# Optimization experiments

Hardware: AMD Instinct MI355X
Metric: run time of the kernel (lower is better)

The kernel has to match this reference:

```python
import jax, jax.numpy as jnp
import numpy as np

SIZE = 1024
M = 10            # log2(SIZE); number of butterfly factors
N_TERMS = 10
BATCH = 8192

# diagonal offset of butterfly j (order matches torch: range(m)[::-1])
DIAGS = [1 << (M - 1 - j) for j in range(M)]


def setup_inputs() -> dict:
    key = jax.random.key(0)
    k1, k2, k3, k4, k5 = jax.random.split(key, 5)
    x = jax.random.normal(k1, (BATCH, SIZE), dtype=jnp.float32)
    diag = jax.random.normal(k2, (M, SIZE), dtype=jnp.float32)
    subpad = jax.random.normal(k3, (M, SIZE), dtype=jnp.float32)
    suppad = jax.random.normal(k4, (M, SIZE), dtype=jnp.float32)
    logit = jax.random.normal(k5, (N_TERMS, M), dtype=jnp.float32)
    # zero the padded positions: subdiag has length SIZE-d stored in [d:],
    # superdiag has length SIZE-d stored in [:-d]
    idx = np.arange(SIZE)
    sub_mask = np.stack([idx >= d for d in DIAGS]).astype(np.float32)
    sup_mask = np.stack([idx < SIZE - d for d in DIAGS]).astype(np.float32)
    subpad = subpad * jnp.asarray(sub_mask)
    suppad = suppad * jnp.asarray(sup_mask)
    return {"x": x, "diag": diag, "subpad": subpad, "suppad": suppad, "logit": logit}


def _butterfly(x, dg, sb, sp, d):
    # out = dg*x; out[d:] += subdiag*x[:-d]; out[:-d] += superdiag*x[d:]
    z = jnp.zeros(x.shape[:-1] + (d,), x.dtype)
    x_right = jnp.concatenate([z, x[..., :-d]], axis=-1)  # x shifted right by d
    x_left = jnp.concatenate([x[..., d:], z], axis=-1)    # x shifted left by d
    return dg * x + sb * x_right + sp * x_left


def reference(x, diag, subpad, suppad, logit):
    prob = jax.nn.softmax(logit, axis=-1)  # (n_terms, m)
    out = x
    for i in range(N_TERMS)[::-1]:
        # apply all m butterflies to current output, stack on last dim
        ys = jnp.stack(
            [_butterfly(out, diag[j], subpad[j], suppad[j], DIAGS[j]) for j in range(M)],
            axis=-1,
        )  # (..., size, m)
        out = jnp.einsum('bsm,m->bs', ys, prob[i])
    return out
```

## Files before the change

### kernel.cpp

```cpp
#include <hip/hip_runtime.h>

#define SIZE 1024
#define MM 10
#define NTERMS 10

typedef _Float16 f16;
typedef __attribute__((ext_vector_type(8))) _Float16 f16x8;
typedef __attribute__((ext_vector_type(4))) _Float16 f16x4;
typedef __attribute__((ext_vector_type(4))) float    f32x4;
typedef __attribute__((ext_vector_type(2))) int      i2;

typedef const __attribute__((address_space(1))) _Float16 gf16;
typedef __attribute__((address_space(3))) _Float16 sf16;

__device__ __forceinline__ float4 ldq(const float* p) { return *(const float4*)p; }

#define FMA4F(W, v0, v1, v2, v3)                                     \
    a0 = fmaf((W)[0], (v0), a0); a1 = fmaf((W)[1], (v1), a1);        \
    a2 = fmaf((W)[2], (v2), a2); a3 = fmaf((W)[3], (v3), a3);

__device__ __forceinline__ void cvt16(const float4& v0, const float4& v1, f16x8& h) {
    h[0] = (f16)v0.x; h[1] = (f16)v0.y; h[2] = (f16)v0.z; h[3] = (f16)v0.w;
    h[4] = (f16)v1.x; h[5] = (f16)v1.y; h[6] = (f16)v1.z; h[7] = (f16)v1.w;
}

__global__ __launch_bounds__(256, 2)
void fused_pre(const float* __restrict__ x,
               const float* __restrict__ diag,
               const float* __restrict__ subpad,
               const float* __restrict__ suppad,
               const float* __restrict__ logit,
               f16* __restrict__ Gt,
               f16* __restrict__ xh)
{
    __shared__ float buf[2][2][SIZE];

    const int tid = threadIdx.x;

    if (blockIdx.x >= 512) {
        const long i = ((long)(blockIdx.x - 512) * 256 + tid) * 16;
        const float4 a = ldq(x + i), b = ldq(x + i + 4),
                     c = ldq(x + i + 8), d = ldq(x + i + 12);
        f16x8 h0, h1; cvt16(a, b, h0); cvt16(c, d, h1);
        *(f16x8*)(xh + i)     = h0;
        *(f16x8*)(xh + i + 8) = h1;
        return;
    }

    const int s0  = tid * 4;
    const int rowbase = blockIdx.x * 2;

    #pragma unroll
    for (int r = 0; r < 2; ++r) {
        float4 v;
        v.x = (rowbase + r == s0 + 0) ? 1.f : 0.f;
        v.y = (rowbase + r == s0 + 1) ? 1.f : 0.f;
        v.z = (rowbase + r == s0 + 2) ? 1.f : 0.f;
        v.w = (rowbase + r == s0 + 3) ? 1.f : 0.f;
        *(float4*)&buf[0][r][s0] = v;
    }
    __syncthreads();

    int cur = 0;
    for (int t = 0; t < NTERMS; ++t) {
        const int i = NTERMS - 1 - t;

        float lg[MM];
        float mx = -3.4e38f;
        #pragma unroll
        for (int j = 0; j < MM; ++j) { lg[j] = logit[i * MM + j]; mx = fmaxf(mx, lg[j]); }
        float ssum = 0.f;
        #pragma unroll
        for (int j = 0; j < MM; ++j) { lg[j] = __expf(lg[j] - mx); ssum += lg[j]; }
        const float inv = 1.0f / ssum;

        float D[4] = {0.f, 0.f, 0.f, 0.f};
        float Wsb[MM][4], Wsp[MM][4];
        #pragma unroll
        for (int j = 0; j < MM; ++j) {
            const float pj = lg[j] * inv;
            const float4 dg = ldq(diag   + j * SIZE + s0);
            const float4 sb = ldq(subpad + j * SIZE + s0);
            const float4 sp = ldq(suppad + j * SIZE + s0);
            D[0] = fmaf(pj, dg.x, D[0]); D[1] = fmaf(pj, dg.y, D[1]);
            D[2] = fmaf(pj, dg.z, D[2]); D[3] = fmaf(pj, dg.w, D[3]);
            Wsb[j][0] = pj * sb.x; Wsb[j][1] = pj * sb.y;
            Wsb[j][2] = pj * sb.z; Wsb[j][3] = pj * sb.w;
            Wsp[j][0] = pj * sp.x; Wsp[j][1] = pj * sp.y;
            Wsp[j][2] = pj * sp.z; Wsp[j][3] = pj * sp.w;
        }

        const bool last = (t == NTERMS - 1);
        for (int r = 0; r < 2; ++r) {
            const float* row = &buf[cur][r][0];

            const float4 xo = ldq(row + s0);
            float a0 = D[0] * xo.x, a1 = D[1] * xo.y,
                  a2 = D[2] * xo.z, a3 = D[3] * xo.w;

            const float4 xl = ldq(row + (s0 >= 4         ? s0 - 4 : 0));
            const float4 xr = ldq(row + (s0 + 4 <= 1020  ? s0 + 4 : 1020));

            FMA4F(Wsb[9], xl.w, xo.x, xo.y, xo.z)
            FMA4F(Wsp[9], xo.y, xo.z, xo.w, xr.x)
            FMA4F(Wsb[8], xl.z, xl.w, xo.x, xo.y)
            FMA4F(Wsp[8], xo.z, xo.w, xr.x, xr.y)
            FMA4F(Wsb[7], xl.x, xl.y, xl.z, xl.w)
            FMA4F(Wsp[7], xr.x, xr.y, xr.z, xr.w)
            #pragma unroll
            for (int j = 0; j <= 6; ++j) {
                const int d = 512 >> j;
                const float4 xm = ldq(row + (s0 >= d        ? s0 - d : 0));
                const float4 xp = ldq(row + (s0 + d <= 1020 ? s0 + d : 1020));
                FMA4F(Wsb[j], xm.x, xm.y, xm.z, xm.w)
                FMA4F(Wsp[j], xp.x, xp.y, xp.z, xp.w)
            }

            if (last) {
                const int k = rowbase + r;
                Gt[(long)(s0 + 0) * SIZE + k] = (f16)a0;
                Gt[(long)(s0 + 1) * SIZE + k] = (f16)a1;
                Gt[(long)(s0 + 2) * SIZE + k] = (f16)a2;
                Gt[(long)(s0 + 3) * SIZE + k] = (f16)a3;
            } else {
                *(float4*)&buf[cur ^ 1][r][s0] = make_float4(a0, a1, a2, a3);
            }
        }
        __syncthreads();
        cur ^= 1;
    }
}

#define NKT 32

__global__ __launch_bounds__(64)
void gemm64(const f16* __restrict__ xh,
            const f16* __restrict__ Gt,
            float* __restrict__ out)
{
    __shared__ f16 Xs[2][64][32];

    const int lane = threadIdx.x;
    const int bm   = blockIdx.x & 127;
    const int bn   = blockIdx.x >> 7;
    const int lr   = lane & 15, lk = lane >> 4;

    const f16* gsrc = xh + (long)(bm * 64 + (lane >> 2)) * 1024 + (lane & 3) * 8;

    const f16* gbase = Gt + (long)(bn * 64 + lr) * 1024 + lk * 8;

    f32x4 acc[4][4];
    #pragma unroll
    for (int mi = 0; mi < 4; ++mi)
        #pragma unroll
        for (int ni = 0; ni < 4; ++ni)
            acc[mi][ni] = (f32x4){0.f, 0.f, 0.f, 0.f};

    f16x8 b0, b1, b2, b3;
    f16x8 c0, c1, c2, c3;

#define STAGE(BUF, KT) {                                                      \
        const f16* gp = gsrc + (KT) * 32;                                     \
        sf16* lp = (sf16*)&Xs[BUF][0][0];                                     \
        __builtin_amdgcn_global_load_lds((gf16*)gp,               lp,        16, 0, 0); \
        __builtin_amdgcn_global_load_lds((gf16*)(gp + 16 * 1024), lp +  512, 16, 0, 0); \
        __builtin_amdgcn_global_load_lds((gf16*)(gp + 32 * 1024), lp + 1024, 16, 0, 0); \
        __builtin_amdgcn_global_load_lds((gf16*)(gp + 48 * 1024), lp + 1536, 16, 0, 0); }
#define LOAD_B(B0, B1, B2, B3, KT) {                                  \
        const f16* gp = gbase + (KT) * 32;                            \
        B0 = *(const f16x8*)(gp);                                     \
        B1 = *(const f16x8*)(gp + 16 * 1024);                         \
        B2 = *(const f16x8*)(gp + 32 * 1024);                         \
        B3 = *(const f16x8*)(gp + 48 * 1024); }
#define COMPUTE(BUF, B0, B1, B2, B3) {                                \
        f16x8 a0 = *(const f16x8*)&Xs[BUF][ 0 + lr][lk * 8];          \
        f16x8 a1 = *(const f16x8*)&Xs[BUF][16 + lr][lk * 8];          \
        f16x8 a2 = *(const f16x8*)&Xs[BUF][32 + lr][lk * 8];          \
        f16x8 a3 = *(const f16x8*)&Xs[BUF][48 + lr][lk * 8];          \
        acc[0][0] = __builtin_amdgcn_mfma_f32_16x16x32_f16(a0, B0, acc[0][0], 0, 0, 0); \
        acc[0][1] = __builtin_amdgcn_mfma_f32_16x16x32_f16(a0, B1, acc[0][1], 0, 0, 0); \
        acc[0][2] = __builtin_amdgcn_mfma_f32_16x16x32_f16(a0, B2, acc[0][2], 0, 0, 0); \
        acc[0][3] = __builtin_amdgcn_mfma_f32_16x16x32_f16(a0, B3, acc[0][3], 0, 0, 0); \
        acc[1][0] = __builtin_amdgcn_mfma_f32_16x16x32_f16(a1, B0, acc[1][0], 0, 0, 0); \
        acc[1][1] = __builtin_amdgcn_mfma_f32_16x16x32_f16(a1, B1, acc[1][1], 0, 0, 0); \
        acc[1][2] = __builtin_amdgcn_mfma_f32_16x16x32_f16(a1, B2, acc[1][2], 0, 0, 0); \
        acc[1][3] = __builtin_amdgcn_mfma_f32_16x16x32_f16(a1, B3, acc[1][3], 0, 0, 0); \
        acc[2][0] = __builtin_amdgcn_mfma_f32_16x16x32_f16(a2, B0, acc[2][0], 0, 0, 0); \
        acc[2][1] = __builtin_amdgcn_mfma_f32_16x16x32_f16(a2, B1, acc[2][1], 0, 0, 0); \
        acc[2][2] = __builtin_amdgcn_mfma_f32_16x16x32_f16(a2, B2, acc[2][2], 0, 0, 0); \
        acc[2][3] = __builtin_amdgcn_mfma_f32_16x16x32_f16(a2, B3, acc[2][3], 0, 0, 0); \
        acc[3][0] = __builtin_amdgcn_mfma_f32_16x16x32_f16(a3, B0, acc[3][0], 0, 0, 0); \
        acc[3][1] = __builtin_amdgcn_mfma_f32_16x16x32_f16(a3, B1, acc[3][1], 0, 0, 0); \
        acc[3][2] = __builtin_amdgcn_mfma_f32_16x16x32_f16(a3, B2, acc[3][2], 0, 0, 0); \
        acc[3][3] = __builtin_amdgcn_mfma_f32_16x16x32_f16(a3, B3, acc[3][3], 0, 0, 0); }

    STAGE(0, 0); LOAD_B(b0, b1, b2, b3, 0);
    __syncthreads();

    #pragma unroll 1
    for (int kt2 = 0; kt2 < NKT / 2; ++kt2) {
        const int kt = kt2 * 2;
        STAGE(1, kt + 1);
        LOAD_B(c0, c1, c2, c3, kt + 1);
        COMPUTE(0, b0, b1, b2, b3);
        __syncthreads();
        if (kt2 < NKT / 2 - 1) {
            STAGE(0, kt + 2);
            LOAD_B(b0, b1, b2, b3, kt + 2);
        }
        COMPUTE(1, c0, c1, c2, c3);
        __syncthreads();
    }

    const long orow0 = (long)bm * 64 + lk * 4;
    const int  ocol0 = bn * 64 + lr;
    #pragma unroll
    for (int mi = 0; mi < 4; ++mi)
        #pragma unroll
        for (int ni = 0; ni < 4; ++ni)
            #pragma unroll
            for (int q = 0; q < 4; ++q)
                out[(orow0 + mi * 16 + q) * 1024 + ocol0 + ni * 16] = acc[mi][ni][q];

#undef STAGE
#undef LOAD_B
#undef COMPUTE
}

#define RPB 16
#define MIX_L(acc, r32, ww) \
    asm("v_fma_mix_f32 %0, %1, %2, %0 op_sel:[0,0,0] op_sel_hi:[1,0,0]" \
        : "+v"(acc) : "v"(r32), "v"(ww))
#define MIX_H(acc, r32, ww) \
    asm("v_fma_mix_f32 %0, %1, %2, %0 op_sel:[1,0,0] op_sel_hi:[1,0,0]" \
        : "+v"(acc) : "v"(r32), "v"(ww))

__global__ __launch_bounds__(256, 2)
void butterfly_h16mix(const float* __restrict__ x,
                      const float* __restrict__ diag,
                      const float* __restrict__ subpad,
                      const float* __restrict__ suppad,
                      const float* __restrict__ logit,
                      float* __restrict__ out)
{
    __shared__ f16 buf[2][RPB][SIZE];
    const int tid = threadIdx.x;
    const int s0  = tid * 4;
    const long rowbase = (long)blockIdx.x * RPB;

    #pragma unroll
    for (int r = 0; r < RPB; ++r) {
        const float4 v = ldq(x + (rowbase + r) * SIZE + s0);
        f16x4 h;
        h[0] = (f16)v.x; h[1] = (f16)v.y; h[2] = (f16)v.z; h[3] = (f16)v.w;
        *(f16x4*)&buf[0][r][s0] = h;
    }
    __syncthreads();

    int cur = 0;
    for (int t = 0; t < NTERMS; ++t) {
        const int i = NTERMS - 1 - t;
        float lg[MM];
        float mx = -3.4e38f;
        #pragma unroll
        for (int j = 0; j < MM; ++j) { lg[j] = logit[i * MM + j]; mx = fmaxf(mx, lg[j]); }
        float ssum = 0.f;
        #pragma unroll
        for (int j = 0; j < MM; ++j) { lg[j] = __expf(lg[j] - mx); ssum += lg[j]; }
        const float inv = 1.0f / ssum;

        float D[4] = {0.f, 0.f, 0.f, 0.f};
        float Wsb[MM][4], Wsp[MM][4];
        #pragma unroll
        for (int j = 0; j < MM; ++j) {
            const float pj = lg[j] * inv;
            const float4 dg = ldq(diag   + j * SIZE + s0);
            const float4 sb = ldq(subpad + j * SIZE + s0);
            const float4 sp = ldq(suppad + j * SIZE + s0);
            D[0] = fmaf(pj, dg.x, D[0]); D[1] = fmaf(pj, dg.y, D[1]);
            D[2] = fmaf(pj, dg.z, D[2]); D[3] = fmaf(pj, dg.w, D[3]);
            Wsb[j][0] = pj * sb.x; Wsb[j][1] = pj * sb.y;
            Wsb[j][2] = pj * sb.z; Wsb[j][3] = pj * sb.w;
            Wsp[j][0] = pj * sp.x; Wsp[j][1] = pj * sp.y;
            Wsp[j][2] = pj * sp.z; Wsp[j][3] = pj * sp.w;
        }

        const bool last = (t == NTERMS - 1);
        for (int r = 0; r < RPB; ++r) {
            const f16* row = &buf[cur][r][0];
            const i2 xo = *(const i2*)&row[s0];
            const i2 xl = *(const i2*)&row[(s0 >= 4)        ? s0 - 4 : 0];
            const i2 xr = *(const i2*)&row[(s0 + 4 <= 1020) ? s0 + 4 : 1020];
            float a0 = 0.f, a1 = 0.f, a2 = 0.f, a3 = 0.f;

            MIX_L(a0, xo.x, D[0]); MIX_H(a1, xo.x, D[1]);
            MIX_L(a2, xo.y, D[2]); MIX_H(a3, xo.y, D[3]);
            MIX_H(a0, xl.y, Wsb[9][0]); MIX_L(a1, xo.x, Wsb[9][1]);
            MIX_H(a2, xo.x, Wsb[9][2]); MIX_L(a3, xo.y, Wsb[9][3]);
            MIX_H(a0, xo.x, Wsp[9][0]); MIX_L(a1, xo.y, Wsp[9][1]);
            MIX_H(a2, xo.y, Wsp[9][2]); MIX_L(a3, xr.x, Wsp[9][3]);
            MIX_L(a0, xl.y, Wsb[8][0]); MIX_H(a1, xl.y, Wsb[8][1]);
            MIX_L(a2, xo.x, Wsb[8][2]); MIX_H(a3, xo.x, Wsb[8][3]);
            MIX_L(a0, xo.y, Wsp[8][0]); MIX_H(a1, xo.y, Wsp[8][1]);
            MIX_L(a2, xr.x, Wsp[8][2]); MIX_H(a3, xr.x, Wsp[8][3]);
            MIX_L(a0, xl.x, Wsb[7][0]); MIX_H(a1, xl.x, Wsb[7][1]);
            MIX_L(a2, xl.y, Wsb[7][2]); MIX_H(a3, xl.y, Wsb[7][3]);
            MIX_L(a0, xr.x, Wsp[7][0]); MIX_H(a1, xr.x, Wsp[7][1]);
            MIX_L(a2, xr.y, Wsp[7][2]); MIX_H(a3, xr.y, Wsp[7][3]);
            #pragma unroll
            for (int j = 0; j <= 6; ++j) {
                const int d = 512 >> j;
                const i2 xm = *(const i2*)&row[(s0 >= d)        ? s0 - d : 0];
                const i2 xp = *(const i2*)&row[(s0 + d <= 1020) ? s0 + d : 1020];
                MIX_L(a0, xm.x, Wsb[j][0]); MIX_H(a1, xm.x, Wsb[j][1]);
                MIX_L(a2, xm.y, Wsb[j][2]); MIX_H(a3, xm.y, Wsb[j][3]);
                MIX_L(a0, xp.x, Wsp[j][0]); MIX_H(a1, xp.x, Wsp[j][1]);
                MIX_L(a2, xp.y, Wsp[j][2]); MIX_H(a3, xp.y, Wsp[j][3]);
            }

            if (last) {
                *(float4*)(out + (rowbase + r) * SIZE + s0) =
                    make_float4(a0, a1, a2, a3);
            } else {
                f16x4 hv;
                hv[0] = (f16)a0; hv[1] = (f16)a1; hv[2] = (f16)a2; hv[3] = (f16)a3;
                *(f16x4*)&buf[cur ^ 1][r][s0] = hv;
            }
        }
        __syncthreads();
        cur ^= 1;
    }
}

extern "C" void kernel_launch(void* const* d_in, const int* in_sizes, int n_in,
                              void* d_out, int out_size, void* d_ws, size_t ws_size,
                              hipStream_t stream) {
    const float* x      = (const float*)d_in[0];
    const float* diag   = (const float*)d_in[1];
    const float* subpad = (const float*)d_in[2];
    const float* suppad = (const float*)d_in[3];
    const float* logit  = (const float*)d_in[4];
    float* outp = (float*)d_out;

    const int batch = in_sizes[0] / SIZE;
    const size_t needGt = (size_t)SIZE * SIZE * sizeof(f16);
    const size_t needXh = (size_t)batch * SIZE * sizeof(f16);

    if (d_ws != nullptr && ws_size >= needGt + needXh) {
        f16* Gt = (f16*)d_ws;
        f16* xh = (f16*)((char*)d_ws + needGt);
        const int cvtBlocks = (int)(((long)batch * SIZE) / (256 * 16));
        fused_pre<<<dim3(512 + cvtBlocks), dim3(256), 0, stream>>>(
            x, diag, subpad, suppad, logit, Gt, xh);
        const int nblocks = (batch / 64) * (SIZE / 64);
        gemm64<<<dim3(nblocks), dim3(64), 0, stream>>>(xh, Gt, outp);
    } else {
        butterfly_h16mix<<<dim3(batch / RPB), dim3(256), 0, stream>>>(
            x, diag, subpad, suppad, logit, outp);
    }
}
```

Baseline: 82.03 us.

## Triple-buffer gemm64 LDS stages with vmcnt waits instead of barriers

```diff
diff --git a/kernel.cpp b/kernel.cpp
--- a/kernel.cpp
+++ b/kernel.cpp
@@ -138,7 +138,7 @@
             const f16* __restrict__ Gt,
             float* __restrict__ out)
 {
-    __shared__ f16 Xs[2][64][32];
+    __shared__ f16 Xs[3][64][32];
 
     const int lane = threadIdx.x;
     const int bm   = blockIdx.x & 127;
@@ -146,7 +146,6 @@
     const int lr   = lane & 15, lk = lane >> 4;
 
     const f16* gsrc = xh + (long)(bm * 64 + (lane >> 2)) * 1024 + (lane & 3) * 8;
-
     const f16* gbase = Gt + (long)(bn * 64 + lr) * 1024 + lk * 8;
 
     f32x4 acc[4][4];
@@ -156,9 +155,14 @@
         for (int ni = 0; ni < 4; ++ni)
             acc[mi][ni] = (f32x4){0.f, 0.f, 0.f, 0.f};
 
-    f16x8 b0, b1, b2, b3;
-    f16x8 c0, c1, c2, c3;
-
+    f16x8 bE0, bE1, bE2, bE3;
+    f16x8 bO0, bO1, bO2, bO3;
+    f16x8 a0, a1, a2, a3;
+
+#define WAITV8 { asm volatile("s_waitcnt vmcnt(8)" ::: "memory"); \
+                 __builtin_amdgcn_sched_barrier(0); }
+#define WAITV4 { asm volatile("s_waitcnt vmcnt(4)" ::: "memory"); \
+                 __builtin_amdgcn_sched_barrier(0); }
 #define STAGE(BUF, KT) {                                                      \
         const f16* gp = gsrc + (KT) * 32;                                     \
         sf16* lp = (sf16*)&Xs[BUF][0][0];                                     \
@@ -166,17 +170,19 @@
         __builtin_amdgcn_global_load_lds((gf16*)(gp + 16 * 1024), lp +  512, 16, 0, 0); \
         __builtin_amdgcn_global_load_lds((gf16*)(gp + 32 * 1024), lp + 1024, 16, 0, 0); \
         __builtin_amdgcn_global_load_lds((gf16*)(gp + 48 * 1024), lp + 1536, 16, 0, 0); }
-#define LOAD_B(B0, B1, B2, B3, KT) {                                  \
+#define LOADB(B0, B1, B2, B3, KT) {                                   \
         const f16* gp = gbase + (KT) * 32;                            \
         B0 = *(const f16x8*)(gp);                                     \
         B1 = *(const f16x8*)(gp + 16 * 1024);                         \
         B2 = *(const f16x8*)(gp + 32 * 1024);                         \
         B3 = *(const f16x8*)(gp + 48 * 1024); }
-#define COMPUTE(BUF, B0, B1, B2, B3) {                                \
-        f16x8 a0 = *(const f16x8*)&Xs[BUF][ 0 + lr][lk * 8];          \
-        f16x8 a1 = *(const f16x8*)&Xs[BUF][16 + lr][lk * 8];          \
-        f16x8 a2 = *(const f16x8*)&Xs[BUF][32 + lr][lk * 8];          \
-        f16x8 a3 = *(const f16x8*)&Xs[BUF][48 + lr][lk * 8];          \
+#define READA(BUF) {                                                  \
+        const f16* base = (const f16*)&Xs[BUF][0][0];                 \
+        a0 = *(const f16x8*)(base + ( 0 + lr) * 32 + lk * 8);         \
+        a1 = *(const f16x8*)(base + (16 + lr) * 32 + lk * 8);         \
+        a2 = *(const f16x8*)(base + (32 + lr) * 32 + lk * 8);         \
+        a3 = *(const f16x8*)(base + (48 + lr) * 32 + lk * 8); }
+#define MFMA16(B0, B1, B2, B3) {                                      \
         acc[0][0] = __builtin_amdgcn_mfma_f32_16x16x32_f16(a0, B0, acc[0][0], 0, 0, 0); \
         acc[0][1] = __builtin_amdgcn_mfma_f32_16x16x32_f16(a0, B1, acc[0][1], 0, 0, 0); \
         acc[0][2] = __builtin_amdgcn_mfma_f32_16x16x32_f16(a0, B2, acc[0][2], 0, 0, 0); \
@@ -194,23 +200,29 @@
         acc[3][2] = __builtin_amdgcn_mfma_f32_16x16x32_f16(a3, B2, acc[3][2], 0, 0, 0); \
         acc[3][3] = __builtin_amdgcn_mfma_f32_16x16x32_f16(a3, B3, acc[3][3], 0, 0, 0); }
 
-    STAGE(0, 0); LOAD_B(b0, b1, b2, b3, 0);
-    __syncthreads();
+    STAGE(0, 0); STAGE(1, 1); LOADB(bE0, bE1, bE2, bE3, 0);
 
     #pragma unroll 1
-    for (int kt2 = 0; kt2 < NKT / 2; ++kt2) {
+    for (int kt2 = 0; kt2 < 15; ++kt2) {
         const int kt = kt2 * 2;
-        STAGE(1, kt + 1);
-        LOAD_B(c0, c1, c2, c3, kt + 1);
-        COMPUTE(0, b0, b1, b2, b3);
-        __syncthreads();
-        if (kt2 < NKT / 2 - 1) {
-            STAGE(0, kt + 2);
-            LOAD_B(b0, b1, b2, b3, kt + 2);
-        }
-        COMPUTE(1, c0, c1, c2, c3);
-        __syncthreads();
-    }
+        WAITV8;
+        READA(kt % 3);
+        STAGE((kt + 2) % 3, kt + 2);
+        LOADB(bO0, bO1, bO2, bO3, kt + 1);
+        MFMA16(bE0, bE1, bE2, bE3);
+        WAITV8;
+        READA((kt + 1) % 3);
+        STAGE((kt + 3) % 3, kt + 3);
+        LOADB(bE0, bE1, bE2, bE3, kt + 2);
+        MFMA16(bO0, bO1, bO2, bO3);
+    }
+    WAITV8;
+    READA(0);
+    LOADB(bO0, bO1, bO2, bO3, 31);
+    MFMA16(bE0, bE1, bE2, bE3);
+    WAITV4;
+    READA(1);
+    MFMA16(bO0, bO1, bO2, bO3);
 
     const long orow0 = (long)bm * 64 + lk * 4;
     const int  ocol0 = bn * 64 + lr;
@@ -222,9 +234,12 @@
             for (int q = 0; q < 4; ++q)
                 out[(orow0 + mi * 16 + q) * 1024 + ocol0 + ni * 16] = acc[mi][ni][q];
 
+#undef WAITV8
+#undef WAITV4
 #undef STAGE
-#undef LOAD_B
-#undef COMPUTE
+#undef LOADB
+#undef READA
+#undef MFMA16
 }
 
 #define RPB 16
```

Result: slower. 83.70 us (+2.0%).

## Use 4-wave 128x128x64 GEMM tiles with XOR-swizzled shared-memory A tiles

Applied to the files above, without the earlier changes.

```diff
diff --git a/kernel.cpp b/kernel.cpp
--- a/kernel.cpp
+++ b/kernel.cpp
@@ -131,23 +131,31 @@
     }
 }
 
-#define NKT 32
-
-__global__ __launch_bounds__(64)
-void gemm64(const f16* __restrict__ xh,
-            const f16* __restrict__ Gt,
-            float* __restrict__ out)
+#define BMT 128
+#define BNT 128
+#define BKT 64
+#define NKT (1024 / BKT)
+
+__global__ __launch_bounds__(256, 2)
+void gemm_f16(const f16* __restrict__ xh,
+              const f16* __restrict__ Gt,
+              float* __restrict__ out)
 {
-    __shared__ f16 Xs[2][64][32];
-
-    const int lane = threadIdx.x;
-    const int bm   = blockIdx.x & 127;
-    const int bn   = blockIdx.x >> 7;
+    __shared__ f16 Xs[2][BMT][BKT];
+
+    const int tid  = threadIdx.x;
+    const int bm   = blockIdx.x & 63;
+    const int bn   = blockIdx.x >> 6;
+    const int w    = tid >> 6, lane = tid & 63;
+    const int wm   = w >> 1,  wn   = w & 1;
     const int lr   = lane & 15, lk = lane >> 4;
-
-    const f16* gsrc = xh + (long)(bm * 64 + (lane >> 2)) * 1024 + (lane & 3) * 8;
-
-    const f16* gbase = Gt + (long)(bn * 64 + lr) * 1024 + lk * 8;
+    const int sw   = lr & 7;
+
+    const int srow = (tid >> 6) * 8 + ((tid >> 3) & 7);
+    const int scol = (((tid & 7) ^ ((tid >> 3) & 7))) * 8;
+    const f16* gsrc = xh + (long)(bm * BMT + srow) * 1024 + scol;
+
+    const f16* gbase = Gt + (long)(bn * BNT + wn * 64 + lr) * 1024 + lk * 8;
 
     f32x4 acc[4][4];
     #pragma unroll
@@ -156,64 +164,92 @@
         for (int ni = 0; ni < 4; ++ni)
             acc[mi][ni] = (f32x4){0.f, 0.f, 0.f, 0.f};
 
-    f16x8 b0, b1, b2, b3;
-    f16x8 c0, c1, c2, c3;
+    f16x8 bE0, bE1, bE2, bE3, bE4, bE5, bE6, bE7;
+    f16x8 bO0, bO1, bO2, bO3, bO4, bO5, bO6, bO7;
 
 #define STAGE(BUF, KT) {                                                      \
-        const f16* gp = gsrc + (KT) * 32;                                     \
-        sf16* lp = (sf16*)&Xs[BUF][0][0];                                     \
+        const f16* gp = gsrc + (KT) * BKT;                                    \
+        sf16* lp = (sf16*)&Xs[0][0][0] + (BUF) * 8192 + (tid >> 6) * 512;     \
         __builtin_amdgcn_global_load_lds((gf16*)gp,               lp,        16, 0, 0); \
-        __builtin_amdgcn_global_load_lds((gf16*)(gp + 16 * 1024), lp +  512, 16, 0, 0); \
-        __builtin_amdgcn_global_load_lds((gf16*)(gp + 32 * 1024), lp + 1024, 16, 0, 0); \
-        __builtin_amdgcn_global_load_lds((gf16*)(gp + 48 * 1024), lp + 1536, 16, 0, 0); }
-#define LOAD_B(B0, B1, B2, B3, KT) {                                  \
-        const f16* gp = gbase + (KT) * 32;                            \
-        B0 = *(const f16x8*)(gp);                                     \
-        B1 = *(const f16x8*)(gp + 16 * 1024);                         \
-        B2 = *(const f16x8*)(gp + 32 * 1024);                         \
-        B3 = *(const f16x8*)(gp + 48 * 1024); }
-#define COMPUTE(BUF, B0, B1, B2, B3) {                                \
-        f16x8 a0 = *(const f16x8*)&Xs[BUF][ 0 + lr][lk * 8];          \
-        f16x8 a1 = *(const f16x8*)&Xs[BUF][16 + lr][lk * 8];          \
-        f16x8 a2 = *(const f16x8*)&Xs[BUF][32 + lr][lk * 8];          \
-        f16x8 a3 = *(const f16x8*)&Xs[BUF][48 + lr][lk * 8];          \
-        acc[0][0] = __builtin_amdgcn_mfma_f32_16x16x32_f16(a0, B0, acc[0][0], 0, 0, 0); \
-        acc[0][1] = __builtin_amdgcn_mfma_f32_16x16x32_f16(a0, B1, acc[0][1], 0, 0, 0); \
-        acc[0][2] = __builtin_amdgcn_mfma_f32_16x16x32_f16(a0, B2, acc[0][2], 0, 0, 0); \
-        acc[0][3] = __builtin_amdgcn_mfma_f32_16x16x32_f16(a0, B3, acc[0][3], 0, 0, 0); \
-        acc[1][0] = __builtin_amdgcn_mfma_f32_16x16x32_f16(a1, B0, acc[1][0], 0, 0, 0); \
-        acc[1][1] = __builtin_amdgcn_mfma_f32_16x16x32_f16(a1, B1, acc[1][1], 0, 0, 0); \
-        acc[1][2] = __builtin_amdgcn_mfma_f32_16x16x32_f16(a1, B2, acc[1][2], 0, 0, 0); \
-        acc[1][3] = __builtin_amdgcn_mfma_f32_16x16x32_f16(a1, B3, acc[1][3], 0, 0, 0); \
-        acc[2][0] = __builtin_amdgcn_mfma_f32_16x16x32_f16(a2, B0, acc[2][0], 0, 0, 0); \
-        acc[2][1] = __builtin_amdgcn_mfma_f32_16x16x32_f16(a2, B1, acc[2][1], 0, 0, 0); \
-        acc[2][2] = __builtin_amdgcn_mfma_f32_16x16x32_f16(a2, B2, acc[2][2], 0, 0, 0); \
-        acc[2][3] = __builtin_amdgcn_mfma_f32_16x16x32_f16(a2, B3, acc[2][3], 0, 0, 0); \
-        acc[3][0] = __builtin_amdgcn_mfma_f32_16x16x32_f16(a3, B0, acc[3][0], 0, 0, 0); \
-        acc[3][1] = __builtin_amdgcn_mfma_f32_16x16x32_f16(a3, B1, acc[3][1], 0, 0, 0); \
-        acc[3][2] = __builtin_amdgcn_mfma_f32_16x16x32_f16(a3, B2, acc[3][2], 0, 0, 0); \
-        acc[3][3] = __builtin_amdgcn_mfma_f32_16x16x32_f16(a3, B3, acc[3][3], 0, 0, 0); }
-
-    STAGE(0, 0); LOAD_B(b0, b1, b2, b3, 0);
+        __builtin_amdgcn_global_load_lds((gf16*)(gp + 32 * 1024), lp + 2048, 16, 0, 0); \
+        __builtin_amdgcn_global_load_lds((gf16*)(gp + 64 * 1024), lp + 4096, 16, 0, 0); \
+        __builtin_amdgcn_global_load_lds((gf16*)(gp + 96 * 1024), lp + 6144, 16, 0, 0); }
+#define LOADB(S, KT) {                                                \
+        const f16* gp = gbase + (KT) * BKT;                           \
+        S##0 = *(const f16x8*)(gp);                                   \
+        S##1 = *(const f16x8*)(gp + 32);                              \
+        S##2 = *(const f16x8*)(gp + 16 * 1024);                       \
+        S##3 = *(const f16x8*)(gp + 16 * 1024 + 32);                  \
+        S##4 = *(const f16x8*)(gp + 32 * 1024);                       \
+        S##5 = *(const f16x8*)(gp + 32 * 1024 + 32);                  \
+        S##6 = *(const f16x8*)(gp + 48 * 1024);                       \
+        S##7 = *(const f16x8*)(gp + 48 * 1024 + 32); }
+#define COMPUTE(BUF, S) {                                                     \
+        const f16* base = (const f16*)&Xs[0][0][0] + (BUF) * 8192;            \
+        const int rb = (wm * 64 + lr) * 64;                                   \
+        const int s0e = ((lk     ^ sw) * 8);                                  \
+        const int s1e = (((4 + lk) ^ sw) * 8);                                \
+        f16x8 a0 = *(const f16x8*)(base + rb +    0      + s0e);              \
+        f16x8 a1 = *(const f16x8*)(base + rb + 16 * 64   + s0e);              \
+        f16x8 a2 = *(const f16x8*)(base + rb + 32 * 64   + s0e);              \
+        f16x8 a3 = *(const f16x8*)(base + rb + 48 * 64   + s0e);              \
+        acc[0][0] = __builtin_amdgcn_mfma_f32_16x16x32_f16(a0, S##0, acc[0][0], 0, 0, 0); \
+        acc[0][1] = __builtin_amdgcn_mfma_f32_16x16x32_f16(a0, S##2, acc[0][1], 0, 0, 0); \
+        acc[0][2] = __builtin_amdgcn_mfma_f32_16x16x32_f16(a0, S##4, acc[0][2], 0, 0, 0); \
+        acc[0][3] = __builtin_amdgcn_mfma_f32_16x16x32_f16(a0, S##6, acc[0][3], 0, 0, 0); \
+        acc[1][0] = __builtin_amdgcn_mfma_f32_16x16x32_f16(a1, S##0, acc[1][0], 0, 0, 0); \
+        acc[1][1] = __builtin_amdgcn_mfma_f32_16x16x32_f16(a1, S##2, acc[1][1], 0, 0, 0); \
+        acc[1][2] = __builtin_amdgcn_mfma_f32_16x16x32_f16(a1, S##4, acc[1][2], 0, 0, 0); \
+        acc[1][3] = __builtin_amdgcn_mfma_f32_16x16x32_f16(a1, S##6, acc[1][3], 0, 0, 0); \
+        acc[2][0] = __builtin_amdgcn_mfma_f32_16x16x32_f16(a2, S##0, acc[2][0], 0, 0, 0); \
+        acc[2][1] = __builtin_amdgcn_mfma_f32_16x16x32_f16(a2, S##2, acc[2][1], 0, 0, 0); \
+        acc[2][2] = __builtin_amdgcn_mfma_f32_16x16x32_f16(a2, S##4, acc[2][2], 0, 0, 0); \
+        acc[2][3] = __builtin_amdgcn_mfma_f32_16x16x32_f16(a2, S##6, acc[2][3], 0, 0, 0); \
+        acc[3][0] = __builtin_amdgcn_mfma_f32_16x16x32_f16(a3, S##0, acc[3][0], 0, 0, 0); \
+        acc[3][1] = __builtin_amdgcn_mfma_f32_16x16x32_f16(a3, S##2, acc[3][1], 0, 0, 0); \
+        acc[3][2] = __builtin_amdgcn_mfma_f32_16x16x32_f16(a3, S##4, acc[3][2], 0, 0, 0); \
+        acc[3][3] = __builtin_amdgcn_mfma_f32_16x16x32_f16(a3, S##6, acc[3][3], 0, 0, 0); \
+        a0 = *(const f16x8*)(base + rb +    0      + s1e);                    \
+        a1 = *(const f16x8*)(base + rb + 16 * 64   + s1e);                    \
+        a2 = *(const f16x8*)(base + rb + 32 * 64   + s1e);                    \
+        a3 = *(const f16x8*)(base + rb + 48 * 64   + s1e);                    \
+        acc[0][0] = __builtin_amdgcn_mfma_f32_16x16x32_f16(a0, S##1, acc[0][0], 0, 0, 0); \
+        acc[0][1] = __builtin_amdgcn_mfma_f32_16x16x32_f16(a0, S##3, acc[0][1], 0, 0, 0); \
+        acc[0][2] = __builtin_amdgcn_mfma_f32_16x16x32_f16(a0, S##5, acc[0][2], 0, 0, 0); \
+        acc[0][3] = __builtin_amdgcn_mfma_f32_16x16x32_f16(a0, S##7, acc[0][3], 0, 0, 0); \
+        acc[1][0] = __builtin_amdgcn_mfma_f32_16x16x32_f16(a1, S##1, acc[1][0], 0, 0, 0); \
+        acc[1][1] = __builtin_amdgcn_mfma_f32_16x16x32_f16(a1, S##3, acc[1][1], 0, 0, 0); \
+        acc[1][2] = __builtin_amdgcn_mfma_f32_16x16x32_f16(a1, S##5, acc[1][2], 0, 0, 0); \
+        acc[1][3] = __builtin_amdgcn_mfma_f32_16x16x32_f16(a1, S##7, acc[1][3], 0, 0, 0); \
+        acc[2][0] = __builtin_amdgcn_mfma_f32_16x16x32_f16(a2, S##1, acc[2][0], 0, 0, 0); \
+        acc[2][1] = __builtin_amdgcn_mfma_f32_16x16x32_f16(a2, S##3, acc[2][1], 0, 0, 0); \
+        acc[2][2] = __builtin_amdgcn_mfma_f32_16x16x32_f16(a2, S##5, acc[2][2], 0, 0, 0); \
+        acc[2][3] = __builtin_amdgcn_mfma_f32_16x16x32_f16(a2, S##7, acc[2][3], 0, 0, 0); \
+        acc[3][0] = __builtin_amdgcn_mfma_f32_16x16x32_f16(a3, S##1, acc[3][0], 0, 0, 0); \
+        acc[3][1] = __builtin_amdgcn_mfma_f32_16x16x32_f16(a3, S##3, acc[3][1], 0, 0, 0); \
+        acc[3][2] = __builtin_amdgcn_mfma_f32_16x16x32_f16(a3, S##5, acc[3][2], 0, 0, 0); \
+        acc[3][3] = __builtin_amdgcn_mfma_f32_16x16x32_f16(a3, S##7, acc[3][3], 0, 0, 0); }
+
+    STAGE(0, 0); LOADB(bE, 0);
     __syncthreads();
 
     #pragma unroll 1
     for (int kt2 = 0; kt2 < NKT / 2; ++kt2) {
         const int kt = kt2 * 2;
         STAGE(1, kt + 1);
-        LOAD_B(c0, c1, c2, c3, kt + 1);
-        COMPUTE(0, b0, b1, b2, b3);
+        LOADB(bO, kt + 1);
+        COMPUTE(0, bE);
         __syncthreads();
         if (kt2 < NKT / 2 - 1) {
             STAGE(0, kt + 2);
-            LOAD_B(b0, b1, b2, b3, kt + 2);
-        }
-        COMPUTE(1, c0, c1, c2, c3);
+            LOADB(bE, kt + 2);
+        }
+        COMPUTE(1, bO);
         __syncthreads();
     }
 
-    const long orow0 = (long)bm * 64 + lk * 4;
-    const int  ocol0 = bn * 64 + lr;
+    const long orow0 = (long)bm * BMT + wm * 64 + lk * 4;
+    const int  ocol0 = bn * BNT + wn * 64 + lr;
     #pragma unroll
     for (int mi = 0; mi < 4; ++mi)
         #pragma unroll
@@ -223,7 +259,7 @@
                 out[(orow0 + mi * 16 + q) * 1024 + ocol0 + ni * 16] = acc[mi][ni][q];
 
 #undef STAGE
-#undef LOAD_B
+#undef LOADB
 #undef COMPUTE
 }
 
@@ -352,8 +388,8 @@
         const int cvtBlocks = (int)(((long)batch * SIZE) / (256 * 16));
         fused_pre<<<dim3(512 + cvtBlocks), dim3(256), 0, stream>>>(
             x, diag, subpad, suppad, logit, Gt, xh);
-        const int nblocks = (batch / 64) * (SIZE / 64);
-        gemm64<<<dim3(nblocks), dim3(64), 0, stream>>>(xh, Gt, outp);
+        const int nblocks = (batch / BMT) * (SIZE / BNT);
+        gemm_f16<<<dim3(nblocks), dim3(256), 0, stream>>>(xh, Gt, outp);
     } else {
         butterfly_h16mix<<<dim3(batch / RPB), dim3(256), 0, stream>>>(
             x, diag, subpad, suppad, logit, outp);
```

New measurement: 82.50 us. About the same (+0.6%).
